# Performance work log

Measured on AMD Instinct MI355X. Metric: run time of the kernel, lower is better.

The kernel has to match this reference:

```python
import jax, jax.numpy as jnp
import numpy as np

N_NODES = 100000


def sage_conv(x, src, dst, w_self, w_nei, b):
    # mean aggregation over incoming edges (src -> dst)
    agg = jax.ops.segment_sum(x[src], dst, num_segments=N_NODES)          # [N, d]
    deg = jax.ops.segment_sum(jnp.ones((src.shape[0], 1), x.dtype), dst,
                              num_segments=N_NODES)                        # [N, 1]
    mean = agg / jnp.maximum(deg, 1.0)
    return x @ w_self + mean @ w_nei + b


def setup_inputs() -> dict:
    key = jax.random.key(0)
    ks = jax.random.split(key, 12)
    d_in, d_hid, d_out = 64, 64, 64
    E = 1600000
    s = lambda d: 1.0 / np.sqrt(d)
    return {
        "x": jax.random.normal(ks[0], (N_NODES, d_in), jnp.float32),
        "edge_index": jax.random.randint(ks[1], (2, E), 0, N_NODES, jnp.int64),
        "w_self1": jax.random.normal(ks[2], (d_in, d_hid), jnp.float32) * s(d_in),
        "w_nei1": jax.random.normal(ks[3], (d_in, d_hid), jnp.float32) * s(d_in),
        "b1": jnp.zeros((d_hid,), jnp.float32),
        "w_self2": jax.random.normal(ks[4], (d_hid, d_hid), jnp.float32) * s(d_hid),
        "w_nei2": jax.random.normal(ks[5], (d_hid, d_hid), jnp.float32) * s(d_hid),
        "b2": jnp.zeros((d_hid,), jnp.float32),
        "w_self3": jax.random.normal(ks[6], (d_hid, d_out), jnp.float32) * s(d_hid),
        "w_nei3": jax.random.normal(ks[7], (d_hid, d_out), jnp.float32) * s(d_hid),
        "b3": jnp.zeros((d_out,), jnp.float32),
    }


def reference(x, edge_index, w_self1, w_nei1, b1, w_self2, w_nei2, b2,
              w_self3, w_nei3, b3):
    src, dst = edge_index[0], edge_index[1]
    h = jax.nn.relu(sage_conv(x, src, dst, w_self1, w_nei1, b1))
    h = jax.nn.relu(sage_conv(h, src, dst, w_self2, w_nei2, b2))
    h = sage_conv(h, src, dst, w_self3, w_nei3, b3)
    return h
```

## Files before the change

kernel.cpp:

```cpp
#include <hip/hip_runtime.h>
#include <hip/hip_bf16.h>

#define PB   512
#define CAP  5120

typedef short bf16x8 __attribute__((ext_vector_type(8)));
typedef float f32x4  __attribute__((ext_vector_type(4)));

__device__ __forceinline__ unsigned short f2bf(float f) {
    unsigned u = __float_as_uint(f);
    u += 0x7FFFu + ((u >> 16) & 1u);
    return (unsigned short)(u >> 16);
}

__global__ __launch_bounds__(256) void build_and_prep(
        const int* __restrict__ src, const int* __restrict__ dst,
        int* __restrict__ gcount, int* __restrict__ pairs, int E, int NB,
        const float* __restrict__ x, unsigned short* __restrict__ xb, int n8,
        const float* __restrict__ Ws1, const float* __restrict__ Wn1,
        const float* __restrict__ Ws2, const float* __restrict__ Wn2,
        const float* __restrict__ Ws3, const float* __restrict__ Wn3,
        unsigned short* __restrict__ bw) {
    const int tid = threadIdx.x;
    if (blockIdx.x < PB) {
        __shared__ int h[512];
        for (int i = tid; i < NB; i += 256) h[i] = 0;
        __syncthreads();
        const int per = (E + PB - 1) / PB;
        const int s = blockIdx.x * per;
        const int e = min(E, s + per);
        for (int i = s + tid; i < e; i += 256) atomicAdd(&h[dst[i] >> 8], 1);
        __syncthreads();
        for (int b = tid; b < NB; b += 256) {
            const int c = h[b];
            h[b] = (c > 0) ? atomicAdd(&gcount[b], c) : 0;
        }
        __syncthreads();
        for (int i = s + tid; i < e; i += 256) {
            const int d = dst[i];
            const int b = d >> 8;
            const int slot = atomicAdd(&h[b], 1);
            if (slot < CAP)
                pairs[(size_t)b * CAP + slot] = src[i] | ((d & 255) << 20);
        }
    } else if (blockIdx.x < PB + 96) {
        const int i = (blockIdx.x - PB) * 256 + tid;
        const int w = i >> 13;
        const int r = i & 8191;
        const float* Ws = (w == 0) ? Ws1 : (w == 1) ? Ws2 : Ws3;
        const float* Wn = (w == 0) ? Wn1 : (w == 1) ? Wn2 : Wn3;
        const int j = r & 7;
        const int L = (r >> 3) & 63;
        const int t = (r >> 9) & 3;
        const int s = r >> 11;
        const int k = s * 32 + ((L >> 4) << 3) + j;
        const int n = t * 16 + (L & 15);
        const float v = (k < 64) ? Ws[k * 64 + n] : Wn[(k - 64) * 64 + n];
        bw[i] = f2bf(v);
    } else {
        const int g = (blockIdx.x - PB - 96) * 256 + tid;
        if (g >= n8) return;
        const float4 v0 = *(const float4*)(x + (size_t)g * 8);
        const float4 v1 = *(const float4*)(x + (size_t)g * 8 + 4);
        uint4 o;
        o.x = (unsigned)f2bf(v0.x) | ((unsigned)f2bf(v0.y) << 16);
        o.y = (unsigned)f2bf(v0.z) | ((unsigned)f2bf(v0.w) << 16);
        o.z = (unsigned)f2bf(v1.x) | ((unsigned)f2bf(v1.y) << 16);
        o.w = (unsigned)f2bf(v1.z) | ((unsigned)f2bf(v1.w) << 16);
        *(uint4*)(xb + (size_t)g * 8) = o;
    }
}

__global__ __launch_bounds__(512) void csr_finalize(const int* __restrict__ pairs,
                                                    const int* __restrict__ gcount,
                                                    int2* __restrict__ rowrange,
                                                    int* __restrict__ col, int N) {
    __shared__ int sp[CAP];
    __shared__ int h[256];
    __shared__ int tmp[256];
    __shared__ int cur[256];
    const int tid = threadIdx.x;
    const int b = blockIdx.x;
    const size_t base = (size_t)b * CAP;
    const int cnt = min(gcount[b], (int)CAP);

    for (int i = tid; i < cnt; i += 512) sp[i] = pairs[base + i];
    if (tid < 256) h[tid] = 0;
    __syncthreads();
    for (int i = tid; i < cnt; i += 512)
        atomicAdd(&h[(sp[i] >> 20) & 255], 1);
    __syncthreads();
    if (tid < 256) tmp[tid] = h[tid];
    __syncthreads();
    for (int off = 1; off < 256; off <<= 1) {
        int t = (tid >= off && tid < 256) ? tmp[tid - off] : 0;
        __syncthreads();
        if (tid < 256) tmp[tid] += t;
        __syncthreads();
    }
    if (tid < 256) {
        const int v = h[tid];
        const int excl = tmp[tid] - v;
        const int node = (b << 8) + tid;
        if (node < N) rowrange[node] = make_int2((int)base + excl, (int)base + excl + v);
        cur[tid] = excl;
    }
    __syncthreads();
    for (int i = tid; i < cnt; i += 512) {
        const int p = sp[i];
        const int slot = atomicAdd(&cur[(p >> 20) & 255], 1);
        col[base + slot] = p & 0xFFFFF;
    }
}

#define ACC8U(A, V)                                                   \
    A[0] += __uint_as_float((V).x << 16);                             \
    A[1] += __uint_as_float((V).x & 0xFFFF0000u);                     \
    A[2] += __uint_as_float((V).y << 16);                             \
    A[3] += __uint_as_float((V).y & 0xFFFF0000u);                     \
    A[4] += __uint_as_float((V).z << 16);                             \
    A[5] += __uint_as_float((V).z & 0xFFFF0000u);                     \
    A[6] += __uint_as_float((V).w << 16);                             \
    A[7] += __uint_as_float((V).w & 0xFFFF0000u);

__global__ __launch_bounds__(128) void sage_fused_kernel(
        const unsigned short* __restrict__ xin, const int* __restrict__ col,
        const int2* __restrict__ rowrange,
        const unsigned short* __restrict__ bswp, const float* __restrict__ bias,
        unsigned short* __restrict__ outb,
        float* __restrict__ outf,
        int N, int do_relu) {
    __shared__ __align__(16) unsigned short smean[32][72];

    const int tid = threadIdx.x;
    const int node0 = blockIdx.x * 32;
    const int lane = tid & 63;

    {
        const int nl = tid >> 2;
        const int node = node0 + nl;
        const int o = (tid & 3) * 8;
        float accA[8] = {0.f}, accB[8] = {0.f};
        float accC[8] = {0.f}, accD[8] = {0.f};
        float rd = 0.f;
        if (node < N) {
            const int2 rr = rowrange[node];
            const int beg = rr.x;
            const int end = rr.y;
            int i = beg;
            for (; i + 4 <= end; i += 4) {
                const int s0 = col[i + 0];
                const int s1 = col[i + 1];
                const int s2 = col[i + 2];
                const int s3 = col[i + 3];
                const unsigned short* p0 = xin + (size_t)s0 * 64 + o;
                const unsigned short* p1 = xin + (size_t)s1 * 64 + o;
                const unsigned short* p2 = xin + (size_t)s2 * 64 + o;
                const unsigned short* p3 = xin + (size_t)s3 * 64 + o;
                const uint4 a0 = *(const uint4*)(p0);
                const uint4 b0 = *(const uint4*)(p0 + 32);
                const uint4 a1 = *(const uint4*)(p1);
                const uint4 b1 = *(const uint4*)(p1 + 32);
                const uint4 a2 = *(const uint4*)(p2);
                const uint4 b2 = *(const uint4*)(p2 + 32);
                const uint4 a3 = *(const uint4*)(p3);
                const uint4 b3 = *(const uint4*)(p3 + 32);
                ACC8U(accA, a0) ACC8U(accB, b0)
                ACC8U(accC, a1) ACC8U(accD, b1)
                ACC8U(accA, a2) ACC8U(accB, b2)
                ACC8U(accC, a3) ACC8U(accD, b3)
            }
            for (; i < end; ++i) {
                const unsigned short* p = xin + (size_t)col[i] * 64 + o;
                const uint4 a = *(const uint4*)(p);
                const uint4 b = *(const uint4*)(p + 32);
                ACC8U(accA, a) ACC8U(accB, b)
            }
            rd = 1.0f / fmaxf((float)(end - beg), 1.0f);
        }
        uint4 o0, o1;
        {
            float m[8];
#pragma unroll
            for (int k = 0; k < 8; ++k) m[k] = (accA[k] + accC[k]) * rd;
            o0.x = (unsigned)f2bf(m[0]) | ((unsigned)f2bf(m[1]) << 16);
            o0.y = (unsigned)f2bf(m[2]) | ((unsigned)f2bf(m[3]) << 16);
            o0.z = (unsigned)f2bf(m[4]) | ((unsigned)f2bf(m[5]) << 16);
            o0.w = (unsigned)f2bf(m[6]) | ((unsigned)f2bf(m[7]) << 16);
#pragma unroll
            for (int k = 0; k < 8; ++k) m[k] = (accB[k] + accD[k]) * rd;
            o1.x = (unsigned)f2bf(m[0]) | ((unsigned)f2bf(m[1]) << 16);
            o1.y = (unsigned)f2bf(m[2]) | ((unsigned)f2bf(m[3]) << 16);
            o1.z = (unsigned)f2bf(m[4]) | ((unsigned)f2bf(m[5]) << 16);
            o1.w = (unsigned)f2bf(m[6]) | ((unsigned)f2bf(m[7]) << 16);
        }
        *(uint4*)(&smean[nl][o])      = o0;
        *(uint4*)(&smean[nl][o + 32]) = o1;
    }
    __syncthreads();

    const int wave = tid >> 6;
    const int m    = lane & 15;
    const int quad = lane >> 4;
    const int nw0  = node0 + wave * 16;

    int arow = nw0 + m;
    if (arow >= N) arow = N - 1;
    const unsigned short* xr = xin + (size_t)arow * 64 + quad * 8;

    f32x4 acc[4];
#pragma unroll
    for (int t = 0; t < 4; ++t) {
        const float b = bias[t * 16 + m];
        acc[t] = (f32x4){b, b, b, b};
    }

#pragma unroll
    for (int s = 0; s < 4; ++s) {
        bf16x8 a;
        if (s < 2) a = *(const bf16x8*)(xr + s * 32);
        else       a = *(const bf16x8*)(&smean[wave * 16 + m][(s - 2) * 32 + quad * 8]);
#pragma unroll
        for (int t = 0; t < 4; ++t) {
            const bf16x8 bf = *(const bf16x8*)(bswp + (((s * 4 + t) * 64 + lane) << 3));
            acc[t] = __builtin_amdgcn_mfma_f32_16x16x32_bf16(a, bf, acc[t], 0, 0, 0);
        }
    }

#pragma unroll
    for (int t = 0; t < 4; ++t) {
        const int colg = t * 16 + m;
#pragma unroll
        for (int r = 0; r < 4; ++r) {
            const int node = nw0 + quad * 4 + r;
            if (node < N) {
                float v = acc[t][r];
                if (do_relu) v = fmaxf(v, 0.f);
                if (outf) outf[(size_t)node * 64 + colg] = v;
                if (outb) outb[(size_t)node * 64 + colg] = f2bf(v);
            }
        }
    }
}

extern "C" void kernel_launch(void* const* d_in, const int* in_sizes, int n_in,
                              void* d_out, int out_size, void* d_ws, size_t ws_size,
                              hipStream_t stream) {
    const float* x   = (const float*)d_in[0];
    const int*   ei  = (const int*)d_in[1];
    const float* ws1 = (const float*)d_in[2];
    const float* wn1 = (const float*)d_in[3];
    const float* b1  = (const float*)d_in[4];
    const float* ws2 = (const float*)d_in[5];
    const float* wn2 = (const float*)d_in[6];
    const float* b2  = (const float*)d_in[7];
    const float* ws3 = (const float*)d_in[8];
    const float* wn3 = (const float*)d_in[9];
    const float* b3  = (const float*)d_in[10];

    const int N = in_sizes[0] / 64;
    const int E = in_sizes[1] / 2;
    const int* src = ei;
    const int* dst = ei + E;
    const int NB = (N + 255) >> 8;

    float* out = (float*)d_out;

    auto align256 = [](size_t v) { return (v + 255) / 256 * 256; };
    char* p = (char*)d_ws;
    int*  gcount   = (int*)p;  p += align256((size_t)NB * 4);
    int*  pairs    = (int*)p;  p += align256((size_t)NB * CAP * 4);
    int*  col      = (int*)p;  p += align256((size_t)NB * CAP * 4);
    int2* rowrange = (int2*)p; p += align256((size_t)N * 8);
    unsigned short* xb  = (unsigned short*)p; p += align256((size_t)N * 64 * 2);
    unsigned short* xb2 = (unsigned short*)p; p += align256((size_t)N * 64 * 2);
    unsigned short* bw  = (unsigned short*)p; p += align256(3 * 8192 * 2);

    const int n8 = N * 64 / 8;
    const int merged_blocks = PB + 96 + (n8 + 255) / 256;
    const int fused_blocks = (N + 31) / 32;

    hipMemsetAsync(gcount, 0, (size_t)NB * 4, stream);
    build_and_prep<<<merged_blocks, 256, 0, stream>>>(src, dst, gcount, pairs, E, NB,
                                                      x, xb, n8,
                                                      ws1, wn1, ws2, wn2, ws3, wn3, bw);
    csr_finalize<<<NB, 512, 0, stream>>>(pairs, gcount, rowrange, col, N);

    sage_fused_kernel<<<fused_blocks, 128, 0, stream>>>(xb,  col, rowrange, bw,         b1, xb2,     nullptr, N, 1);
    sage_fused_kernel<<<fused_blocks, 128, 0, stream>>>(xb2, col, rowrange, bw + 8192,  b2, xb,      nullptr, N, 1);
    sage_fused_kernel<<<fused_blocks, 128, 0, stream>>>(xb,  col, rowrange, bw + 16384, b3, nullptr, out,     N, 0);
}
```

Before: 256.8 us.

## Replace binned CSR build with fixed-capacity per-node adjacency slots

After: 357.7 us. 39.3% more time.

```diff
diff --git a/kernel.cpp b/kernel.cpp
--- a/kernel.cpp
+++ b/kernel.cpp
@@ -1,8 +1,7 @@
 #include <hip/hip_runtime.h>
 #include <hip/hip_bf16.h>
 
-#define PB   512
-#define CAP  5120
+#define RCAP 64
 
 typedef short bf16x8 __attribute__((ext_vector_type(8)));
 typedef float f32x4  __attribute__((ext_vector_type(4)));
@@ -15,36 +14,24 @@
 
 __global__ __launch_bounds__(256) void build_and_prep(
         const int* __restrict__ src, const int* __restrict__ dst,
-        int* __restrict__ gcount, int* __restrict__ pairs, int E, int NB,
+        int* __restrict__ cnt, int* __restrict__ col, int E,
         const float* __restrict__ x, unsigned short* __restrict__ xb, int n8,
         const float* __restrict__ Ws1, const float* __restrict__ Wn1,
         const float* __restrict__ Ws2, const float* __restrict__ Wn2,
         const float* __restrict__ Ws3, const float* __restrict__ Wn3,
         unsigned short* __restrict__ bw) {
     const int tid = threadIdx.x;
-    if (blockIdx.x < PB) {
-        __shared__ int h[512];
-        for (int i = tid; i < NB; i += 256) h[i] = 0;
-        __syncthreads();
-        const int per = (E + PB - 1) / PB;
-        const int s = blockIdx.x * per;
-        const int e = min(E, s + per);
-        for (int i = s + tid; i < e; i += 256) atomicAdd(&h[dst[i] >> 8], 1);
-        __syncthreads();
-        for (int b = tid; b < NB; b += 256) {
-            const int c = h[b];
-            h[b] = (c > 0) ? atomicAdd(&gcount[b], c) : 0;
-        }
-        __syncthreads();
-        for (int i = s + tid; i < e; i += 256) {
+    const int EB = (E + 255) >> 8;
+    if (blockIdx.x < EB) {
+        const int i = blockIdx.x * 256 + tid;
+        if (i < E) {
             const int d = dst[i];
-            const int b = d >> 8;
-            const int slot = atomicAdd(&h[b], 1);
-            if (slot < CAP)
-                pairs[(size_t)b * CAP + slot] = src[i] | ((d & 255) << 20);
-        }
-    } else if (blockIdx.x < PB + 96) {
-        const int i = (blockIdx.x - PB) * 256 + tid;
+            const int s = src[i];
+            const int slot = atomicAdd(&cnt[d], 1);
+            if (slot < RCAP) col[(size_t)d * RCAP + slot] = s;
+        }
+    } else if (blockIdx.x < EB + 96) {
+        const int i = (blockIdx.x - EB) * 256 + tid;
         const int w = i >> 13;
         const int r = i & 8191;
         const float* Ws = (w == 0) ? Ws1 : (w == 1) ? Ws2 : Ws3;
@@ -58,7 +45,7 @@
         const float v = (k < 64) ? Ws[k * 64 + n] : Wn[(k - 64) * 64 + n];
         bw[i] = f2bf(v);
     } else {
-        const int g = (blockIdx.x - PB - 96) * 256 + tid;
+        const int g = (blockIdx.x - EB - 96) * 256 + tid;
         if (g >= n8) return;
         const float4 v0 = *(const float4*)(x + (size_t)g * 8);
         const float4 v1 = *(const float4*)(x + (size_t)g * 8 + 4);
@@ -71,48 +58,6 @@
     }
 }
 
-__global__ __launch_bounds__(512) void csr_finalize(const int* __restrict__ pairs,
-                                                    const int* __restrict__ gcount,
-                                                    int2* __restrict__ rowrange,
-                                                    int* __restrict__ col, int N) {
-    __shared__ int sp[CAP];
-    __shared__ int h[256];
-    __shared__ int tmp[256];
-    __shared__ int cur[256];
-    const int tid = threadIdx.x;
-    const int b = blockIdx.x;
-    const size_t base = (size_t)b * CAP;
-    const int cnt = min(gcount[b], (int)CAP);
-
-    for (int i = tid; i < cnt; i += 512) sp[i] = pairs[base + i];
-    if (tid < 256) h[tid] = 0;
-    __syncthreads();
-    for (int i = tid; i < cnt; i += 512)
-        atomicAdd(&h[(sp[i] >> 20) & 255], 1);
-    __syncthreads();
-    if (tid < 256) tmp[tid] = h[tid];
-    __syncthreads();
-    for (int off = 1; off < 256; off <<= 1) {
-        int t = (tid >= off && tid < 256) ? tmp[tid - off] : 0;
-        __syncthreads();
-        if (tid < 256) tmp[tid] += t;
-        __syncthreads();
-    }
-    if (tid < 256) {
-        const int v = h[tid];
-        const int excl = tmp[tid] - v;
-        const int node = (b << 8) + tid;
-        if (node < N) rowrange[node] = make_int2((int)base + excl, (int)base + excl + v);
-        cur[tid] = excl;
-    }
-    __syncthreads();
-    for (int i = tid; i < cnt; i += 512) {
-        const int p = sp[i];
-        const int slot = atomicAdd(&cur[(p >> 20) & 255], 1);
-        col[base + slot] = p & 0xFFFFF;
-    }
-}
-
 #define ACC8U(A, V)                                                   \
     A[0] += __uint_as_float((V).x << 16);                             \
     A[1] += __uint_as_float((V).x & 0xFFFF0000u);                     \
@@ -123,9 +68,9 @@
     A[6] += __uint_as_float((V).w << 16);                             \
     A[7] += __uint_as_float((V).w & 0xFFFF0000u);
 
-__global__ __launch_bounds__(128) void sage_fused_kernel(
+__global__ __launch_bounds__(256) void sage_fused_kernel(
         const unsigned short* __restrict__ xin, const int* __restrict__ col,
-        const int2* __restrict__ rowrange,
+        const int* __restrict__ cnts,
         const unsigned short* __restrict__ bswp, const float* __restrict__ bias,
         unsigned short* __restrict__ outb,
         float* __restrict__ outf,
@@ -137,104 +82,99 @@
     const int lane = tid & 63;
 
     {
-        const int nl = tid >> 2;
+        const int nl = tid >> 3;
         const int node = node0 + nl;
-        const int o = (tid & 3) * 8;
-        float accA[8] = {0.f}, accB[8] = {0.f};
-        float accC[8] = {0.f}, accD[8] = {0.f};
+        const int o = (tid & 7) * 8;
+        float acc0[8] = {0.f}, acc1[8] = {0.f};
         float rd = 0.f;
         if (node < N) {
-            const int2 rr = rowrange[node];
-            const int beg = rr.x;
-            const int end = rr.y;
-            int i = beg;
-            for (; i + 4 <= end; i += 4) {
-                const int s0 = col[i + 0];
-                const int s1 = col[i + 1];
-                const int s2 = col[i + 2];
-                const int s3 = col[i + 3];
-                const unsigned short* p0 = xin + (size_t)s0 * 64 + o;
-                const unsigned short* p1 = xin + (size_t)s1 * 64 + o;
-                const unsigned short* p2 = xin + (size_t)s2 * 64 + o;
-                const unsigned short* p3 = xin + (size_t)s3 * 64 + o;
-                const uint4 a0 = *(const uint4*)(p0);
-                const uint4 b0 = *(const uint4*)(p0 + 32);
-                const uint4 a1 = *(const uint4*)(p1);
-                const uint4 b1 = *(const uint4*)(p1 + 32);
-                const uint4 a2 = *(const uint4*)(p2);
-                const uint4 b2 = *(const uint4*)(p2 + 32);
-                const uint4 a3 = *(const uint4*)(p3);
-                const uint4 b3 = *(const uint4*)(p3 + 32);
-                ACC8U(accA, a0) ACC8U(accB, b0)
-                ACC8U(accC, a1) ACC8U(accD, b1)
-                ACC8U(accA, a2) ACC8U(accB, b2)
-                ACC8U(accC, a3) ACC8U(accD, b3)
-            }
-            for (; i < end; ++i) {
-                const unsigned short* p = xin + (size_t)col[i] * 64 + o;
-                const uint4 a = *(const uint4*)(p);
-                const uint4 b = *(const uint4*)(p + 32);
-                ACC8U(accA, a) ACC8U(accB, b)
-            }
-            rd = 1.0f / fmaxf((float)(end - beg), 1.0f);
-        }
-        uint4 o0, o1;
-        {
-            float m[8];
-#pragma unroll
-            for (int k = 0; k < 8; ++k) m[k] = (accA[k] + accC[k]) * rd;
-            o0.x = (unsigned)f2bf(m[0]) | ((unsigned)f2bf(m[1]) << 16);
-            o0.y = (unsigned)f2bf(m[2]) | ((unsigned)f2bf(m[3]) << 16);
-            o0.z = (unsigned)f2bf(m[4]) | ((unsigned)f2bf(m[5]) << 16);
-            o0.w = (unsigned)f2bf(m[6]) | ((unsigned)f2bf(m[7]) << 16);
-#pragma unroll
-            for (int k = 0; k < 8; ++k) m[k] = (accB[k] + accD[k]) * rd;
-            o1.x = (unsigned)f2bf(m[0]) | ((unsigned)f2bf(m[1]) << 16);
-            o1.y = (unsigned)f2bf(m[2]) | ((unsigned)f2bf(m[3]) << 16);
-            o1.z = (unsigned)f2bf(m[4]) | ((unsigned)f2bf(m[5]) << 16);
-            o1.w = (unsigned)f2bf(m[6]) | ((unsigned)f2bf(m[7]) << 16);
-        }
-        *(uint4*)(&smean[nl][o])      = o0;
-        *(uint4*)(&smean[nl][o + 32]) = o1;
+            const int cnt = min(cnts[node], RCAP);
+            const int beg = node * RCAP;
+            int i = 0;
+            for (; i + 8 <= cnt; i += 8) {
+                int s[8];
+#pragma unroll
+                for (int k = 0; k < 8; ++k) s[k] = col[beg + i + k];
+                uint4 v[8];
+#pragma unroll
+                for (int k = 0; k < 8; ++k)
+                    v[k] = *(const uint4*)(xin + (size_t)s[k] * 64 + o);
+#pragma unroll
+                for (int k = 0; k < 8; k += 2) {
+                    ACC8U(acc0, v[k]) ACC8U(acc1, v[k + 1])
+                }
+            }
+            if (i + 4 <= cnt) {
+                int s[4];
+#pragma unroll
+                for (int k = 0; k < 4; ++k) s[k] = col[beg + i + k];
+                uint4 v[4];
+#pragma unroll
+                for (int k = 0; k < 4; ++k)
+                    v[k] = *(const uint4*)(xin + (size_t)s[k] * 64 + o);
+#pragma unroll
+                for (int k = 0; k < 4; k += 2) {
+                    ACC8U(acc0, v[k]) ACC8U(acc1, v[k + 1])
+                }
+                i += 4;
+            }
+            for (; i < cnt; ++i) {
+                const uint4 v = *(const uint4*)(xin + (size_t)col[beg + i] * 64 + o);
+                ACC8U(acc0, v)
+            }
+            rd = 1.0f / fmaxf((float)cnt, 1.0f);
+        }
+        float m[8];
+#pragma unroll
+        for (int k = 0; k < 8; ++k) m[k] = (acc0[k] + acc1[k]) * rd;
+        uint4 ov;
+        ov.x = (unsigned)f2bf(m[0]) | ((unsigned)f2bf(m[1]) << 16);
+        ov.y = (unsigned)f2bf(m[2]) | ((unsigned)f2bf(m[3]) << 16);
+        ov.z = (unsigned)f2bf(m[4]) | ((unsigned)f2bf(m[5]) << 16);
+        ov.w = (unsigned)f2bf(m[6]) | ((unsigned)f2bf(m[7]) << 16);
+        *(uint4*)(&smean[nl][o]) = ov;
     }
     __syncthreads();
 
     const int wave = tid >> 6;
     const int m    = lane & 15;
     const int quad = lane >> 4;
-    const int nw0  = node0 + wave * 16;
+    const int nh   = wave & 1;
+    const int th   = wave >> 1;
+    const int nw0  = node0 + nh * 16;
 
     int arow = nw0 + m;
     if (arow >= N) arow = N - 1;
     const unsigned short* xr = xin + (size_t)arow * 64 + quad * 8;
 
-    f32x4 acc[4];
-#pragma unroll
-    for (int t = 0; t < 4; ++t) {
-        const float b = bias[t * 16 + m];
-        acc[t] = (f32x4){b, b, b, b};
+    f32x4 acc[2];
+#pragma unroll
+    for (int j = 0; j < 2; ++j) {
+        const float b = bias[(th * 2 + j) * 16 + m];
+        acc[j] = (f32x4){b, b, b, b};
     }
 
 #pragma unroll
     for (int s = 0; s < 4; ++s) {
         bf16x8 a;
         if (s < 2) a = *(const bf16x8*)(xr + s * 32);
-        else       a = *(const bf16x8*)(&smean[wave * 16 + m][(s - 2) * 32 + quad * 8]);
-#pragma unroll
-        for (int t = 0; t < 4; ++t) {
+        else       a = *(const bf16x8*)(&smean[nh * 16 + m][(s - 2) * 32 + quad * 8]);
+#pragma unroll
+        for (int j = 0; j < 2; ++j) {
+            const int t = th * 2 + j;
             const bf16x8 bf = *(const bf16x8*)(bswp + (((s * 4 + t) * 64 + lane) << 3));
-            acc[t] = __builtin_amdgcn_mfma_f32_16x16x32_bf16(a, bf, acc[t], 0, 0, 0);
-        }
-    }
-
-#pragma unroll
-    for (int t = 0; t < 4; ++t) {
-        const int colg = t * 16 + m;
+            acc[j] = __builtin_amdgcn_mfma_f32_16x16x32_bf16(a, bf, acc[j], 0, 0, 0);
+        }
+    }
+
+#pragma unroll
+    for (int j = 0; j < 2; ++j) {
+        const int colg = (th * 2 + j) * 16 + m;
 #pragma unroll
         for (int r = 0; r < 4; ++r) {
             const int node = nw0 + quad * 4 + r;
             if (node < N) {
-                float v = acc[t][r];
+                float v = acc[j][r];
                 if (do_relu) v = fmaxf(v, 0.f);
                 if (outf) outf[(size_t)node * 64 + colg] = v;
                 if (outb) outb[(size_t)node * 64 + colg] = f2bf(v);
@@ -262,31 +202,28 @@
     const int E = in_sizes[1] / 2;
     const int* src = ei;
     const int* dst = ei + E;
-    const int NB = (N + 255) >> 8;
 
     float* out = (float*)d_out;
 
     auto align256 = [](size_t v) { return (v + 255) / 256 * 256; };
     char* p = (char*)d_ws;
-    int*  gcount   = (int*)p;  p += align256((size_t)NB * 4);
-    int*  pairs    = (int*)p;  p += align256((size_t)NB * CAP * 4);
-    int*  col      = (int*)p;  p += align256((size_t)NB * CAP * 4);
-    int2* rowrange = (int2*)p; p += align256((size_t)N * 8);
+    int*  cnt = (int*)p;  p += align256((size_t)N * 4);
+    int*  col = (int*)p;  p += align256((size_t)N * RCAP * 4);
     unsigned short* xb  = (unsigned short*)p; p += align256((size_t)N * 64 * 2);
     unsigned short* xb2 = (unsigned short*)p; p += align256((size_t)N * 64 * 2);
     unsigned short* bw  = (unsigned short*)p; p += align256(3 * 8192 * 2);
 
     const int n8 = N * 64 / 8;
-    const int merged_blocks = PB + 96 + (n8 + 255) / 256;
+    const int EB = (E + 255) >> 8;
+    const int merged_blocks = EB + 96 + (n8 + 255) / 256;
     const int fused_blocks = (N + 31) / 32;
 
-    hipMemsetAsync(gcount, 0, (size_t)NB * 4, stream);
-    build_and_prep<<<merged_blocks, 256, 0, stream>>>(src, dst, gcount, pairs, E, NB,
+    hipMemsetAsync(cnt, 0, (size_t)N * 4, stream);
+    build_and_prep<<<merged_blocks, 256, 0, stream>>>(src, dst, cnt, col, E,
                                                       x, xb, n8,
                                                       ws1, wn1, ws2, wn2, ws3, wn3, bw);
-    csr_finalize<<<NB, 512, 0, stream>>>(pairs, gcount, rowrange, col, N);
-
-    sage_fused_kernel<<<fused_blocks, 128, 0, stream>>>(xb,  col, rowrange, bw,         b1, xb2,     nullptr, N, 1);
-    sage_fused_kernel<<<fused_blocks, 128, 0, stream>>>(xb2, col, rowrange, bw + 8192,  b2, xb,      nullptr, N, 1);
-    sage_fused_kernel<<<fused_blocks, 128, 0, stream>>>(xb,  col, rowrange, bw + 16384, b3, nullptr, out,     N, 0);
-}
+
+    sage_fused_kernel<<<fused_blocks, 256, 0, stream>>>(xb,  col, cnt, bw,         b1, xb2,     nullptr, N, 1);
+    sage_fused_kernel<<<fused_blocks, 256, 0, stream>>>(xb2, col, cnt, bw + 8192,  b2, xb,      nullptr, N, 1);
+    sage_fused_kernel<<<fused_blocks, 256, 0, stream>>>(xb,  col, cnt, bw + 16384, b3, nullptr, out,     N, 0);
+}
```
